# Optimization experiments

Hardware: AMD Instinct MI355X
Metric: run time of the kernel (lower is better)

Reference implementation:

```python
import jax, jax.numpy as jnp
import numpy as np

B, S, C = 4, 2048, 2048
D = C // 4  # head dim = 512

def setup_inputs() -> dict:
    key = jax.random.key(0)
    k1, k2, k3, k4, k5 = jax.random.split(key, 5)
    scale = 1.0 / np.sqrt(C)
    return {
        "x": jax.random.normal(k1, (B, S, C), dtype=jnp.float32),
        "Wqkv": jax.random.normal(k2, (3 * D, C), dtype=jnp.float32) * scale,
        "bqkv": jax.random.normal(k3, (3 * D,), dtype=jnp.float32) * 0.01,
        "Wo": jax.random.normal(k4, (C, D), dtype=jnp.float32) * (1.0 / np.sqrt(D)),
        "bo": jax.random.normal(k5, (C,), dtype=jnp.float32) * 0.01,
    }

def reference(x, Wqkv, bqkv, Wo, bo):
    Bx, Sx, Cx = x.shape
    d = Cx // 4
    # fused QKV projection: [B,S,3d] -> split into q,k,v each [B,S,d]
    qkv = jnp.einsum('bsc,oc->bso', x, Wqkv) + bqkv
    qkv = qkv.reshape(Bx, Sx, 3, d)
    q, k, v = qkv[:, :, 0], qkv[:, :, 1], qkv[:, :, 2]
    # scaled dot-product attention (full [B,S,S] scores, as in original)
    attn = jnp.einsum('bqd,bkd->bqk', q, k) / jnp.sqrt(jnp.asarray(d, x.dtype))
    attn = jax.nn.softmax(attn, axis=-1)
    ctx = jnp.einsum('bqk,bkd->bqd', attn, v)
    # output projection d -> C
    return jnp.einsum('bsd,od->bso', ctx, Wo) + bo
```

## Files before the change

### kernel.cpp

```cpp
#include <hip/hip_runtime.h>
#include <math.h>


typedef __bf16 bf16;
typedef bf16 bf16x8 __attribute__((ext_vector_type(8)));
typedef bf16 bf16x4 __attribute__((ext_vector_type(4)));
typedef float f32x4 __attribute__((ext_vector_type(4)));

#define BB 4
#define SS 2048
#define CC 2048
#define DD 512
#define ND3 1536
#define MM 8192

typedef const __attribute__((address_space(1))) unsigned int g_u32;
typedef __attribute__((address_space(3))) unsigned int l_u32;

__device__ __forceinline__ void gl_lds16(const bf16* g, bf16* l) {
    __builtin_amdgcn_global_load_lds((g_u32*)g, (l_u32*)l, 16, 0, 0);
}

#define N4_X   (MM * CC / 4)
#define N4_WQ  (ND3 * CC / 4)
#define N4_WO  (CC * DD / 4)
#define N4_RS  (MM / 4)
#define N4_TOT (N4_X + N4_WQ + N4_WO + N4_RS)

__global__ __launch_bounds__(256) void prep(const float* __restrict__ x,
                                            const float* __restrict__ Wqkv,
                                            const float* __restrict__ Wo,
                                            bf16* __restrict__ xb,
                                            bf16* __restrict__ wqkvb,
                                            bf16* __restrict__ wob,
                                            float* __restrict__ rsum) {
    int i = blockIdx.x * 256 + threadIdx.x;
    const int stride = gridDim.x * 256;
    for (; i < N4_TOT; i += stride) {
        if (i < N4_X + N4_WQ + N4_WO) {
            const float* src; bf16* dst; int j = i;
            if (j < N4_X)                { src = x;    dst = xb; }
            else if (j < N4_X + N4_WQ)   { src = Wqkv; dst = wqkvb; j -= N4_X; }
            else                         { src = Wo;   dst = wob;   j -= N4_X + N4_WQ; }
            float4 v = ((const float4*)src)[j];
            bf16x4 o;
            o[0] = (bf16)v.x; o[1] = (bf16)v.y; o[2] = (bf16)v.z; o[3] = (bf16)v.w;
            ((bf16x4*)dst)[j] = o;
        } else {
            int j = i - (N4_X + N4_WQ + N4_WO);
            ((float4*)rsum)[j] = float4{0.f, 0.f, 0.f, 0.f};
        }
    }
}

template <bool OUT_BF16, int BN, int EPI>
__device__ __forceinline__ void gemm_body(const bf16* __restrict__ A,
                                          const bf16* __restrict__ Bm,
                                          const float* __restrict__ bias,
                                          float* __restrict__ rowsum,
                                          bf16* __restrict__ vTp,
                                          void* __restrict__ Cv,
                                          int K, int lda, int ldb, int ldc,
                                          long ab, long bb, long cb,
                                          float scale) {
    constexpr int TM = (BN == 128) ? 4 : 2;
    constexpr int NB = (BN == 128) ? 4 : 2;
    __shared__ bf16 As[128 * 64];
    __shared__ bf16 Bs[BN * 64];
    A += (size_t)blockIdx.z * ab;
    Bm += (size_t)blockIdx.z * bb;
    const int m0 = blockIdx.y * 128, n0 = blockIdx.x * BN;
    const int t = threadIdx.x, lane = t & 63, w = t >> 6;
    const int wm = (BN == 128) ? (w >> 1) * 64 : w * 32;
    const int wn = (BN == 128) ? (w & 1) * 64 : 0;
    const int q = lane >> 4, cl = lane & 15;
    const int srow = lane >> 3;
    const int sblk = (lane & 7) ^ srow;
    const int scol = sblk * 8;
    const bf16* pa = A + (size_t)(m0 + w * 32 + srow) * lda + scol;
    const int brow0 = (BN == 128) ? w * 32 : w * 16;
    const bf16* pb = Bm + (size_t)(n0 + brow0 + srow) * ldb + scol;
    bf16* lA = As + (w * 32) * 64;
    bf16* lB = Bs + brow0 * 64;
    const int rblk0 = (q ^ (cl & 7)) * 8;
    const int rblk1 = ((4 + q) ^ (cl & 7)) * 8;

    f32x4 acc[TM][4] = {};
    for (int k0 = 0; k0 < K; k0 += 64) {
#pragma unroll
        for (int n = 0; n < 4; n++)
            gl_lds16(pa + k0 + (size_t)(n * 8) * lda, lA + n * 8 * 64);
#pragma unroll
        for (int n = 0; n < NB; n++)
            gl_lds16(pb + k0 + (size_t)(n * 8) * ldb, lB + n * 8 * 64);
        __syncthreads();
#pragma unroll
        for (int h = 0; h < 2; h++) {
            const int rb = h ? rblk1 : rblk0;
            bf16x8 af[TM], bfr[4];
#pragma unroll
            for (int i = 0; i < TM; i++)
                af[i] = *(const bf16x8*)&As[(wm + i * 16 + cl) * 64 + rb];
#pragma unroll
            for (int j = 0; j < 4; j++)
                bfr[j] = *(const bf16x8*)&Bs[(wn + j * 16 + cl) * 64 + rb];
#pragma unroll
            for (int i = 0; i < TM; i++)
#pragma unroll
                for (int j = 0; j < 4; j++)
                    acc[i][j] = __builtin_amdgcn_mfma_f32_16x16x32_bf16(af[i], bfr[j], acc[i][j], 0, 0, 0);
        }
        __syncthreads();
    }

    if constexpr (EPI == 4 || EPI == 5) {
        float inv[4], cs[4] = {0.f, 0.f, 0.f, 0.f};
        if constexpr (EPI == 5) {
#pragma unroll
            for (int j = 0; j < 4; j++)
                inv[j] = 1.0f / rowsum[(size_t)blockIdx.z * SS + n0 + wn + j * 16 + cl];
        }
#pragma unroll
        for (int i = 0; i < TM; i++)
#pragma unroll
            for (int j = 0; j < 4; j++) {
                int col = n0 + wn + j * 16 + cl;
                int row = m0 + wm + i * 16 + q * 4;
                bf16x4 o;
                if constexpr (EPI == 4) {
#pragma unroll
                    for (int r = 0; r < 4; r++) {
                        float e = __expf(acc[i][j][r] * scale);
                        cs[j] += e;
                        o[r] = (bf16)e;
                    }
                } else {
#pragma unroll
                    for (int r = 0; r < 4; r++) o[r] = (bf16)(acc[i][j][r] * inv[j]);
                }
                *(bf16x4*)&((bf16*)Cv)[(size_t)blockIdx.z * cb + (size_t)col * ldc + row] = o;
            }
        if constexpr (EPI == 4) {
#pragma unroll
            for (int j = 0; j < 4; j++) {
                cs[j] += __shfl_xor(cs[j], 16, 64);
                cs[j] += __shfl_xor(cs[j], 32, 64);
            }
            if (q == 0) {
#pragma unroll
                for (int j = 0; j < 4; j++)
                    atomicAdd(&rowsum[(size_t)blockIdx.z * SS + n0 + wn + j * 16 + cl], cs[j]);
            }
        }
        return;
    }

    const bool v_block = (EPI == 3) && (n0 >= 1024);
#pragma unroll
    for (int i = 0; i < TM; i++) {
#pragma unroll
        for (int j = 0; j < 4; j++) {
            int col = n0 + wn + j * 16 + cl;
            float bvv = bias ? bias[col] : 0.0f;
            if (v_block) {
                int row = m0 + wm + i * 16 + q * 4;
                int b = row >> 11, s = row & 2047;
                bf16x4 o;
#pragma unroll
                for (int r = 0; r < 4; r++) o[r] = (bf16)(acc[i][j][r] * scale + bvv);
                *(bf16x4*)&vTp[((size_t)b * DD + (col - 1024)) * SS + s] = o;
            } else {
#pragma unroll
                for (int r = 0; r < 4; r++) {
                    int row = m0 + wm + i * 16 + q * 4 + r;
                    float val = acc[i][j][r] * scale + bvv;
                    if (OUT_BF16)
                        ((bf16*)Cv)[(size_t)blockIdx.z * cb + (size_t)row * ldc + col] = (bf16)val;
                    else
                        ((float*)Cv)[(size_t)blockIdx.z * cb + (size_t)row * ldc + col] = val;
                }
            }
        }
    }
}

__global__ __launch_bounds__(256) void k_qkv(const bf16* A, const bf16* Bm,
        const float* bias, bf16* vTp, void* Cv, int K, int lda, int ldb, int ldc,
        float scale) {
    gemm_body<true, 128, 3>(A, Bm, bias, nullptr, vTp, Cv, K, lda, ldb, ldc, 0, 0, 0, scale);
}
__global__ __launch_bounds__(256) void k_score(const bf16* A, const bf16* Bm,
        float* rowsum, void* Cv, int K, int lda, int ldb, int ldc,
        long ab, long bb, long cb, float scale) {
    gemm_body<true, 128, 4>(A, Bm, nullptr, rowsum, nullptr, Cv, K, lda, ldb, ldc, ab, bb, cb, scale);
}
__global__ __launch_bounds__(256) void k_pv(const bf16* A, const bf16* Bm,
        float* rowsum, void* Cv, int K, int lda, int ldb, int ldc,
        long ab, long bb, long cb, float scale) {
    gemm_body<true, 64, 5>(A, Bm, nullptr, rowsum, nullptr, Cv, K, lda, ldb, ldc, ab, bb, cb, scale);
}
__global__ __launch_bounds__(256) void k_out(const bf16* A, const bf16* Bm,
        const float* bias, void* Cv, int K, int lda, int ldb, int ldc,
        float scale) {
    gemm_body<false, 128, 0>(A, Bm, bias, nullptr, nullptr, Cv, K, lda, ldb, ldc, 0, 0, 0, scale);
}

extern "C" void kernel_launch(void* const* d_in, const int* in_sizes, int n_in,
                              void* d_out, int out_size, void* d_ws, size_t ws_size,
                              hipStream_t stream) {
    const float* x    = (const float*)d_in[0];
    const float* Wqkv = (const float*)d_in[1];
    const float* bqkv = (const float*)d_in[2];
    const float* Wo   = (const float*)d_in[3];
    const float* bo   = (const float*)d_in[4];
    float* out = (float*)d_out;

    char* ws = (char*)d_ws;
    size_t off = 0;
    bf16* xb    = (bf16*)(ws + off); off += (size_t)MM * CC * 2;
    bf16* wqkvb = (bf16*)(ws + off); off += (size_t)ND3 * CC * 2;
    bf16* wob   = (bf16*)(ws + off); off += (size_t)CC * DD * 2;
    bf16* qkvb  = (bf16*)(ws + off); off += (size_t)MM * ND3 * 2;
    bf16* vT    = (bf16*)(ws + off); off += (size_t)BB * DD * SS * 2;
    bf16* expS  = (bf16*)(ws + off); off += (size_t)BB * SS * SS * 2;
    bf16* ctxb  = (bf16*)(ws + off); off += (size_t)MM * DD * 2;
    float* rsum = (float*)(ws + off); off += (size_t)MM * 4;

    prep<<<2048, 256, 0, stream>>>(x, Wqkv, Wo, xb, wqkvb, wob, rsum);

    k_qkv<<<dim3(ND3 / 128, MM / 128, 1), 256, 0, stream>>>(
        xb, wqkvb, bqkv, vT, qkvb, CC, CC, CC, ND3, 1.0f);

    k_score<<<dim3(SS / 128, SS / 128, BB), 256, 0, stream>>>(
        qkvb + 512 , qkvb , rsum, expS,
        DD, ND3, ND3, SS,
        (long)SS * ND3, (long)SS * ND3, (long)SS * SS,
        0.044194173824159216f );

    k_pv<<<dim3(SS / 64, DD / 128, BB), 256, 0, stream>>>(
        vT, expS, rsum, ctxb,
        SS, SS, SS, DD,
        (long)DD * SS, (long)SS * SS, (long)SS * DD, 1.0f);

    k_out<<<dim3(CC / 128, MM / 128, 1), 256, 0, stream>>>(
        ctxb, wob, bo, out, DD, DD, DD, CC, 1.0f);

    (void)in_sizes; (void)n_in; (void)out_size; (void)ws_size;
}
```

Before: 306.3 us.

## Use 256x256-tile, 8-wave GEMM with 4-slot LDS pipeline for QKV/score/out

Adds a new GEMM body with 256x256 output tiles computed by 512 threads (8 waves, each owning a 128x64 sub-tile), fed by a 4-slot global_load_lds ring buffer of 128 KB of dynamic LDS with three stages in flight. QKV, score and output projections switch to this body, while PV keeps the old 128-wide path. The goal is more operand reuse per LDS byte, fewer global loads, and latency hidden by deeper prefetch. In exchange the grids have fewer blocks (for example 6x32 for QKV), only one block fits per CU because of the LDS size, register pressure rises, and the launch_bounds(512,2) hint may not be met.

```diff
diff --git a/kernel.cpp b/kernel.cpp
--- a/kernel.cpp
+++ b/kernel.cpp
@@ -49,6 +49,149 @@
         } else {
             int j = i - (N4_X + N4_WQ + N4_WO);
             ((float4*)rsum)[j] = float4{0.f, 0.f, 0.f, 0.f};
+        }
+    }
+}
+
+#define SLOT_E 16384
+#define CH_B   8192
+
+template <bool OUT_BF16, int EPI>
+__device__ __forceinline__ void gemm256_body(const bf16* __restrict__ A,
+                                             const bf16* __restrict__ Bm,
+                                             const float* __restrict__ bias,
+                                             float* __restrict__ rowsum,
+                                             bf16* __restrict__ vTp,
+                                             void* __restrict__ Cv,
+                                             int K, int lda, int ldb, int ldc,
+                                             long ab, long bb, long cb,
+                                             float scale) {
+    extern __shared__ bf16 lds[];
+    A  += (size_t)blockIdx.z * ab;
+    Bm += (size_t)blockIdx.z * bb;
+    const int m0 = blockIdx.y * 256, n0 = blockIdx.x * 256;
+    const int t = threadIdx.x, lane = t & 63, w = t >> 6;
+    const int wm = (w >> 2) * 128, wn = (w & 3) * 64;
+    const int cl = lane & 15, q = lane >> 4;
+    const int swzr = (q ^ ((cl >> 1) & 3)) * 8;
+    const int srow = t >> 2;
+    const int swz  = (t & 3) ^ ((t >> 3) & 3);
+    const bf16* pa = A  + (size_t)(m0 + srow) * lda + swz * 8;
+    const bf16* pb = Bm + (size_t)(n0 + srow) * ldb + swz * 8;
+    bf16* lw = lds + w * 512;
+
+    f32x4 acc[8][4] = {};
+    const int NC = K >> 5;
+
+    auto STAGE = [&](int j) {
+        bf16* s = lw + (j & 3) * SLOT_E;
+        const bf16* ga = pa + j * 32;
+        const bf16* gb = pb + j * 32;
+        gl_lds16(ga,                     s);
+        gl_lds16(ga + (size_t)128 * lda, s + 4096);
+        gl_lds16(gb,                     s + CH_B);
+        gl_lds16(gb + (size_t)128 * ldb, s + CH_B + 4096);
+    };
+    auto FRAGS = [&](int j, bf16x8 (&af)[8], bf16x8 (&bfr)[4]) {
+        const bf16* sa = lds + (j & 3) * SLOT_E + (wm + cl) * 32 + swzr;
+        const bf16* sb = lds + (j & 3) * SLOT_E + CH_B + (wn + cl) * 32 + swzr;
+#pragma unroll
+        for (int i = 0; i < 8; i++)  af[i]  = *(const bf16x8*)(sa + i * 512);
+#pragma unroll
+        for (int jj = 0; jj < 4; jj++) bfr[jj] = *(const bf16x8*)(sb + jj * 512);
+    };
+    auto MFMAS = [&](bf16x8 (&af)[8], bf16x8 (&bfr)[4]) {
+        __builtin_amdgcn_s_setprio(1);
+#pragma unroll
+        for (int i = 0; i < 8; i++)
+#pragma unroll
+            for (int jj = 0; jj < 4; jj++)
+                acc[i][jj] = __builtin_amdgcn_mfma_f32_16x16x32_bf16(
+                                 af[i], bfr[jj], acc[i][jj], 0, 0, 0);
+        __builtin_amdgcn_s_setprio(0);
+    };
+
+    STAGE(0); STAGE(1); STAGE(2);
+    asm volatile("s_waitcnt vmcnt(8)" ::: "memory");
+    __builtin_amdgcn_s_barrier();
+
+    for (int j = 0; j < NC - 3; ++j) {
+        bf16x8 af[8], bfr[4];
+        FRAGS(j, af, bfr);
+        STAGE(j + 3);
+        MFMAS(af, bfr);
+        asm volatile("s_waitcnt vmcnt(8)" ::: "memory");
+        __builtin_amdgcn_s_barrier();
+    }
+    {   bf16x8 af[8], bfr[4];
+        FRAGS(NC - 3, af, bfr); MFMAS(af, bfr);
+        asm volatile("s_waitcnt vmcnt(4)" ::: "memory");
+        __builtin_amdgcn_s_barrier();
+    }
+    {   bf16x8 af[8], bfr[4];
+        FRAGS(NC - 2, af, bfr); MFMAS(af, bfr);
+        asm volatile("s_waitcnt vmcnt(0)" ::: "memory");
+        __builtin_amdgcn_s_barrier();
+    }
+    {   bf16x8 af[8], bfr[4];
+        FRAGS(NC - 1, af, bfr); MFMAS(af, bfr);
+    }
+
+    if constexpr (EPI == 4) {
+        float cs[4] = {0.f, 0.f, 0.f, 0.f};
+#pragma unroll
+        for (int i = 0; i < 8; i++)
+#pragma unroll
+            for (int jj = 0; jj < 4; jj++) {
+                int col = n0 + wn + jj * 16 + cl;
+                int row = m0 + wm + i * 16 + q * 4;
+                bf16x4 o;
+#pragma unroll
+                for (int r = 0; r < 4; r++) {
+                    float e = __expf(acc[i][jj][r] * scale);
+                    cs[jj] += e;
+                    o[r] = (bf16)e;
+                }
+                *(bf16x4*)&((bf16*)Cv)[(size_t)blockIdx.z * cb + (size_t)col * ldc + row] = o;
+            }
+#pragma unroll
+        for (int jj = 0; jj < 4; jj++) {
+            cs[jj] += __shfl_xor(cs[jj], 16, 64);
+            cs[jj] += __shfl_xor(cs[jj], 32, 64);
+        }
+        if (q == 0) {
+#pragma unroll
+            for (int jj = 0; jj < 4; jj++)
+                atomicAdd(&rowsum[(size_t)blockIdx.z * SS + n0 + wn + jj * 16 + cl], cs[jj]);
+        }
+        return;
+    }
+
+    const bool v_block = (EPI == 3) && (n0 >= 1024);
+#pragma unroll
+    for (int i = 0; i < 8; i++) {
+#pragma unroll
+        for (int jj = 0; jj < 4; jj++) {
+            int col = n0 + wn + jj * 16 + cl;
+            float bvv = bias ? bias[col] : 0.0f;
+            if (v_block) {
+                int row = m0 + wm + i * 16 + q * 4;
+                int b = row >> 11, s = row & 2047;
+                bf16x4 o;
+#pragma unroll
+                for (int r = 0; r < 4; r++) o[r] = (bf16)(acc[i][jj][r] * scale + bvv);
+                *(bf16x4*)&vTp[((size_t)b * DD + (col - 1024)) * SS + s] = o;
+            } else {
+#pragma unroll
+                for (int r = 0; r < 4; r++) {
+                    int row = m0 + wm + i * 16 + q * 4 + r;
+                    float val = acc[i][jj][r] * scale + bvv;
+                    if (OUT_BF16)
+                        ((bf16*)Cv)[(size_t)blockIdx.z * cb + (size_t)row * ldc + col] = (bf16)val;
+                    else
+                        ((float*)Cv)[(size_t)blockIdx.z * cb + (size_t)row * ldc + col] = val;
+                }
+            }
         }
     }
 }
@@ -154,55 +297,27 @@
         }
         return;
     }
-
-    const bool v_block = (EPI == 3) && (n0 >= 1024);
-#pragma unroll
-    for (int i = 0; i < TM; i++) {
-#pragma unroll
-        for (int j = 0; j < 4; j++) {
-            int col = n0 + wn + j * 16 + cl;
-            float bvv = bias ? bias[col] : 0.0f;
-            if (v_block) {
-                int row = m0 + wm + i * 16 + q * 4;
-                int b = row >> 11, s = row & 2047;
-                bf16x4 o;
-#pragma unroll
-                for (int r = 0; r < 4; r++) o[r] = (bf16)(acc[i][j][r] * scale + bvv);
-                *(bf16x4*)&vTp[((size_t)b * DD + (col - 1024)) * SS + s] = o;
-            } else {
-#pragma unroll
-                for (int r = 0; r < 4; r++) {
-                    int row = m0 + wm + i * 16 + q * 4 + r;
-                    float val = acc[i][j][r] * scale + bvv;
-                    if (OUT_BF16)
-                        ((bf16*)Cv)[(size_t)blockIdx.z * cb + (size_t)row * ldc + col] = (bf16)val;
-                    else
-                        ((float*)Cv)[(size_t)blockIdx.z * cb + (size_t)row * ldc + col] = val;
-                }
-            }
-        }
-    }
-}
-
-__global__ __launch_bounds__(256) void k_qkv(const bf16* A, const bf16* Bm,
+}
+
+__global__ __launch_bounds__(512, 2) void k_qkv(const bf16* A, const bf16* Bm,
         const float* bias, bf16* vTp, void* Cv, int K, int lda, int ldb, int ldc,
         float scale) {
-    gemm_body<true, 128, 3>(A, Bm, bias, nullptr, vTp, Cv, K, lda, ldb, ldc, 0, 0, 0, scale);
-}
-__global__ __launch_bounds__(256) void k_score(const bf16* A, const bf16* Bm,
+    gemm256_body<true, 3>(A, Bm, bias, nullptr, vTp, Cv, K, lda, ldb, ldc, 0, 0, 0, scale);
+}
+__global__ __launch_bounds__(512, 2) void k_score(const bf16* A, const bf16* Bm,
         float* rowsum, void* Cv, int K, int lda, int ldb, int ldc,
         long ab, long bb, long cb, float scale) {
-    gemm_body<true, 128, 4>(A, Bm, nullptr, rowsum, nullptr, Cv, K, lda, ldb, ldc, ab, bb, cb, scale);
+    gemm256_body<true, 4>(A, Bm, nullptr, rowsum, nullptr, Cv, K, lda, ldb, ldc, ab, bb, cb, scale);
 }
 __global__ __launch_bounds__(256) void k_pv(const bf16* A, const bf16* Bm,
         float* rowsum, void* Cv, int K, int lda, int ldb, int ldc,
         long ab, long bb, long cb, float scale) {
     gemm_body<true, 64, 5>(A, Bm, nullptr, rowsum, nullptr, Cv, K, lda, ldb, ldc, ab, bb, cb, scale);
 }
-__global__ __launch_bounds__(256) void k_out(const bf16* A, const bf16* Bm,
+__global__ __launch_bounds__(512, 2) void k_out(const bf16* A, const bf16* Bm,
         const float* bias, void* Cv, int K, int lda, int ldb, int ldc,
         float scale) {
-    gemm_body<false, 128, 0>(A, Bm, bias, nullptr, nullptr, Cv, K, lda, ldb, ldc, 0, 0, 0, scale);
+    gemm256_body<false, 0>(A, Bm, bias, nullptr, nullptr, Cv, K, lda, ldb, ldc, 0, 0, 0, scale);
 }
 
 extern "C" void kernel_launch(void* const* d_in, const int* in_sizes, int n_in,
@@ -226,12 +341,23 @@
     bf16* ctxb  = (bf16*)(ws + off); off += (size_t)MM * DD * 2;
     float* rsum = (float*)(ws + off); off += (size_t)MM * 4;
 
+    static int lds_attr_set = 0;
+    if (!lds_attr_set) {
+        hipFuncSetAttribute((const void*)k_qkv,
+                            hipFuncAttributeMaxDynamicSharedMemorySize, 131072);
+        hipFuncSetAttribute((const void*)k_score,
+                            hipFuncAttributeMaxDynamicSharedMemorySize, 131072);
+        hipFuncSetAttribute((const void*)k_out,
+                            hipFuncAttributeMaxDynamicSharedMemorySize, 131072);
+        lds_attr_set = 1;
+    }
+
     prep<<<2048, 256, 0, stream>>>(x, Wqkv, Wo, xb, wqkvb, wob, rsum);
 
-    k_qkv<<<dim3(ND3 / 128, MM / 128, 1), 256, 0, stream>>>(
+    k_qkv<<<dim3(ND3 / 256, MM / 256, 1), 512, 131072, stream>>>(
         xb, wqkvb, bqkv, vT, qkvb, CC, CC, CC, ND3, 1.0f);
 
-    k_score<<<dim3(SS / 128, SS / 128, BB), 256, 0, stream>>>(
+    k_score<<<dim3(SS / 256, SS / 256, BB), 512, 131072, stream>>>(
         qkvb + 512 , qkvb , rsum, expS,
         DD, ND3, ND3, SS,
         (long)SS * ND3, (long)SS * ND3, (long)SS * SS,
@@ -242,7 +368,7 @@
         SS, SS, SS, DD,
         (long)DD * SS, (long)SS * SS, (long)SS * DD, 1.0f);
 
-    k_out<<<dim3(CC / 128, MM / 128, 1), 256, 0, stream>>>(
+    k_out<<<dim3(CC / 256, MM / 256, 1), 512, 131072, stream>>>(
         ctxb, wob, bo, out, DD, DD, DD, CC, 1.0f);
 
     (void)in_sizes; (void)n_in; (void)out_size; (void)ws_size;
```

Result: faster. 283.2 us (-7.6%).
